# Optimization experiments

Measured on AMD Instinct MI355X. Metric: run time of the kernel, lower is better.

## Reference

```python
import jax, jax.numpy as jnp
import numpy as np

N_NODES = 100000
N_EDGES = 1000000
F_IN = 64
F_HID = 64
F_OUT = 2
NUM_GRAPHS = 64


def setup_inputs() -> dict:
    key = jax.random.key(0)
    ks = jax.random.split(key, 8)
    x = jax.random.normal(ks[0], (N_NODES, F_IN), dtype=jnp.float32)
    edge_index = jax.random.randint(ks[1], (2, N_EDGES), 0, N_NODES, dtype=jnp.int32)
    batch = jnp.sort(jax.random.randint(ks[2], (N_NODES,), 0, NUM_GRAPHS, dtype=jnp.int32))
    s1 = 1.0 / np.sqrt(F_IN)
    s2 = 1.0 / np.sqrt(F_HID)
    W1 = jax.random.normal(ks[3], (F_IN, F_HID), dtype=jnp.float32) * s1
    W2 = jax.random.normal(ks[4], (F_HID, F_HID), dtype=jnp.float32) * s2
    W3 = jax.random.normal(ks[5], (F_HID, F_HID), dtype=jnp.float32) * s2
    Wlin = jax.random.normal(ks[6], (F_HID, F_OUT), dtype=jnp.float32) * s2
    return {
        "x": x, "edge_index": edge_index, "batch": batch,
        "W1": W1, "b1": jnp.zeros((F_HID,), jnp.float32),
        "W2": W2, "b2": jnp.zeros((F_HID,), jnp.float32),
        "W3": W3, "b3": jnp.zeros((F_HID,), jnp.float32),
        "Wlin": Wlin, "blin": jnp.zeros((F_OUT,), jnp.float32),
    }


def _gcn_norm(edge_index, n_nodes):
    # add self-loops, compute symmetric D^-1/2 (A+I) D^-1/2 edge weights
    loops = jnp.arange(n_nodes, dtype=edge_index.dtype)
    src = jnp.concatenate([edge_index[0], loops])  # message source j
    dst = jnp.concatenate([edge_index[1], loops])  # aggregation target i
    deg = jax.ops.segment_sum(jnp.ones_like(dst, dtype=jnp.float32), dst,
                              num_segments=n_nodes)
    dinv = jnp.where(deg > 0, jax.lax.rsqrt(deg), 0.0)
    norm = dinv[src] * dinv[dst]  # [E+N]
    return src, dst, norm


def _gcn_conv(h, W, b, src, dst, norm, n_nodes):
    h = h @ W                                    # [N, F] dense transform first (PyG order)
    msg = h[src] * norm[:, None]                 # gather + scale  [E+N, F]
    agg = jax.ops.segment_sum(msg, dst, num_segments=n_nodes)
    return agg + b


def reference(x, edge_index, batch, W1, b1, W2, b2, W3, b3, Wlin, blin):
    n = x.shape[0]
    src, dst, norm = _gcn_norm(edge_index, n)
    h = jax.nn.relu(_gcn_conv(x, W1, b1, src, dst, norm, n))
    h = jax.nn.relu(_gcn_conv(h, W2, b2, src, dst, norm, n))
    h = _gcn_conv(h, W3, b3, src, dst, norm, n)
    # global mean pool over graphs
    sums = jax.ops.segment_sum(h, batch, num_segments=NUM_GRAPHS)        # [G, F]
    cnts = jax.ops.segment_sum(jnp.ones((n,), jnp.float32), batch,
                               num_segments=NUM_GRAPHS)
    pooled = sums / jnp.maximum(cnts, 1.0)[:, None]
    # dropout(p=0.1) is identity in eval mode
    return pooled @ Wlin + blin
```

## Files before the change

kernel.cpp:

```cpp
#include <hip/hip_runtime.h>

#define FDIM 64

typedef unsigned short u16;
typedef unsigned int u32;
typedef float v2f __attribute__((ext_vector_type(2)));

__device__ __forceinline__ u16 f2bf(float x) {
    unsigned int u = __float_as_uint(x);
    return (u16)((u + 0x7fff + ((u >> 16) & 1)) >> 16);
}
__device__ __forceinline__ float bf2f(u16 h) {
    return __uint_as_float(((unsigned int)h) << 16);
}
__device__ __forceinline__ u32 pk_fp8x4(float a, float b, float c, float d) {
    u32 p = __builtin_amdgcn_cvt_pk_fp8_f32(a, b, 0, false);
    p = __builtin_amdgcn_cvt_pk_fp8_f32(c, d, p, true);
    return p;
}


template <bool BF16IN>
__device__ __forceinline__ void mm_tile64(
    const void* __restrict__ ain, const float* __restrict__ bias, int do_relu,
    u32* __restrict__ t, int n, int blk,
    float (*__restrict__ As)[FDIM + 1], float* __restrict__ Ws)
{
    int tid = threadIdx.x;
    int r0 = blk * 64;

    #pragma unroll
    for (int i = 0; i < 4; ++i) {
        int idx = tid + 256 * i;
        int r = idx >> 4;
        int kq = idx & 15;
        float4 v = make_float4(0.f, 0.f, 0.f, 0.f);
        int R = r0 + r;
        if (R < n) {
            if (BF16IN) {
                ushort4 h = ((const ushort4*)ain)[(size_t)R * 16 + kq];
                v.x = bf2f(h.x); v.y = bf2f(h.y); v.z = bf2f(h.z); v.w = bf2f(h.w);
            } else {
                v = ((const float4*)ain)[(size_t)R * 16 + kq];
            }
            if (bias != nullptr) {
                float4 b = ((const float4*)bias)[kq];
                v.x += b.x; v.y += b.y; v.z += b.z; v.w += b.w;
            }
            if (do_relu) {
                v.x = fmaxf(v.x, 0.f); v.y = fmaxf(v.y, 0.f);
                v.z = fmaxf(v.z, 0.f); v.w = fmaxf(v.w, 0.f);
            }
        }
        As[r][kq * 4 + 0] = v.x;
        As[r][kq * 4 + 1] = v.y;
        As[r][kq * 4 + 2] = v.z;
        As[r][kq * 4 + 3] = v.w;
    }
    __syncthreads();

    int rq = tid >> 4;
    int cq = tid & 15;
    float acc[4][4];
    #pragma unroll
    for (int i = 0; i < 4; ++i)
        #pragma unroll
        for (int j = 0; j < 4; ++j) acc[i][j] = 0.f;

    const float4* Ws4 = (const float4*)Ws;
    #pragma unroll 4
    for (int k = 0; k < FDIM; ++k) {
        float4 w = Ws4[k * 16 + cq];
        float a[4];
        #pragma unroll
        for (int i = 0; i < 4; ++i) a[i] = As[rq * 4 + i][k];
        #pragma unroll
        for (int i = 0; i < 4; ++i) {
            acc[i][0] = fmaf(a[i], w.x, acc[i][0]);
            acc[i][1] = fmaf(a[i], w.y, acc[i][1]);
            acc[i][2] = fmaf(a[i], w.z, acc[i][2]);
            acc[i][3] = fmaf(a[i], w.w, acc[i][3]);
        }
    }

    #pragma unroll
    for (int i = 0; i < 4; ++i) {
        int R = r0 + rq * 4 + i;
        if (R < n)
            t[(size_t)R * 16 + cq] =
                pk_fp8x4(acc[i][0], acc[i][1], acc[i][2], acc[i][3]);
    }
}

__global__ __launch_bounds__(256) void k_matmul_h(
    const u16* __restrict__ ain, const float* __restrict__ Wm,
    const float* __restrict__ bias, u32* __restrict__ t, int n)
{
    __shared__ float As[64][FDIM + 1];
    __shared__ float Ws[FDIM * FDIM];
    int tid = threadIdx.x;
    #pragma unroll
    for (int i = 0; i < 4; ++i)
        ((float4*)Ws)[tid + 256 * i] = ((const float4*)Wm)[tid + 256 * i];
    mm_tile64<true>(ain, bias, 1, t, n, blockIdx.x, As, Ws);
}


__global__ __launch_bounds__(256) void k_mm_fill(
    const float* __restrict__ x, const float* __restrict__ W1,
    u32* __restrict__ t,
    const int* __restrict__ src, const int* __restrict__ dst,
    int* __restrict__ cnt, int* __restrict__ csr,
    int n, int E, int cap, int mm_blocks, int fill_chunks)
{
    __shared__ float As[64][FDIM + 1];
    __shared__ float Ws[FDIM * FDIM];

    if ((int)blockIdx.x < mm_blocks) {
        int tid = threadIdx.x;
        #pragma unroll
        for (int i = 0; i < 4; ++i)
            ((float4*)Ws)[tid + 256 * i] = ((const float4*)W1)[tid + 256 * i];
        mm_tile64<false>(x, nullptr, 0, t, n, blockIdx.x, As, Ws);
        return;
    }
    int gb = blockIdx.x - mm_blocks;
    int part = blockIdx.x & 7;
    int chunk = gb >> 3;
    int psz = n >> 3;
    int lo = psz * part;
    int hi = (part == 7) ? n : lo + psz;
    int per = (E + fill_chunks - 1) / fill_chunks;
    int ebeg = chunk * per;
    int eend = ebeg + per; if (eend > E) eend = E;

    int e = ebeg + (int)threadIdx.x;
    for (; e + 1792 < eend; e += 2048) {
        int d[8], s[8], p[8];
        bool kk[8];
        #pragma unroll
        for (int u = 0; u < 8; ++u) d[u] = __builtin_nontemporal_load(&dst[e + 256 * u]);
        #pragma unroll
        for (int u = 0; u < 8; ++u) s[u] = __builtin_nontemporal_load(&src[e + 256 * u]);
        #pragma unroll
        for (int u = 0; u < 8; ++u) kk[u] = (d[u] >= lo) && (d[u] < hi);
        #pragma unroll
        for (int u = 0; u < 8; ++u) { p[u] = 0; if (kk[u]) p[u] = atomicAdd(&cnt[d[u]], 1); }
        #pragma unroll
        for (int u = 0; u < 8; ++u)
            if (kk[u] && p[u] < cap) csr[(size_t)d[u] * cap + p[u]] = s[u];
    }
    for (; e < eend; e += 256) {
        int d = dst[e];
        if (d >= lo && d < hi) {
            int p = atomicAdd(&cnt[d], 1);
            if (p < cap) csr[(size_t)d * cap + p] = src[e];
        }
    }
}


__global__ __launch_bounds__(256) void k_aggregate(
    const int* __restrict__ cnt, const int* __restrict__ csr,
    const u32* __restrict__ t, uint2* __restrict__ aggh, int n, int cap)
{
    int tid = threadIdx.x;
    long long gw = ((long long)blockIdx.x * 256 + tid) >> 6;
    int lane = tid & 63;
    int sub = lane >> 4;
    int li  = lane & 15;
    long long il = gw * 4 + sub;
    if (il >= n) return;
    int i = (int)il;

    int deg = cnt[i];
    float di = rsqrtf((float)deg + 1.0f);
    int m = deg < cap ? deg : cap;

    u32 sp = t[(size_t)i * 16 + li];
    v2f s0 = __builtin_amdgcn_cvt_pk_f32_fp8(sp, false);
    v2f s1 = __builtin_amdgcn_cvt_pk_f32_fp8(sp, true);
    float4 A0 = make_float4(s0.x * di, s0.y * di, s1.x * di, s1.y * di);
    float4 A1 = make_float4(0.f, 0.f, 0.f, 0.f);
    float4 A2 = make_float4(0.f, 0.f, 0.f, 0.f);
    float4 A3 = make_float4(0.f, 0.f, 0.f, 0.f);

    const int* row = csr + (size_t)i * cap;
    int nbase = sub << 4;

    for (int c0 = 0; c0 < m; c0 += 16) {
        int cm = m - c0; if (cm > 16) cm = 16;
        int sv = 0; float dvv = 0.f;
        if (li < cm) {
            sv = __builtin_nontemporal_load(&row[c0 + li]);
            dvv = rsqrtf((float)cnt[sv] + 1.0f);
        }
        int k = 0;
        for (; k + 8 <= cm; k += 8) {
            int jv[8]; float dj[8]; u32 v[8];
            #pragma unroll
            for (int u = 0; u < 8; ++u) {
                jv[u] = __shfl(sv, nbase + k + u);
                dj[u] = __shfl(dvv, nbase + k + u);
            }
            #pragma unroll
            for (int u = 0; u < 8; ++u) v[u] = t[(size_t)jv[u] * 16 + li];
            #pragma unroll
            for (int u = 0; u < 8; ++u) {
                v2f x0 = __builtin_amdgcn_cvt_pk_f32_fp8(v[u], false);
                v2f x1 = __builtin_amdgcn_cvt_pk_f32_fp8(v[u], true);
                float4* Ap = (u & 3) == 0 ? &A0 : (u & 3) == 1 ? &A1 :
                             (u & 3) == 2 ? &A2 : &A3;
                Ap->x = fmaf(x0.x, dj[u], Ap->x);
                Ap->y = fmaf(x0.y, dj[u], Ap->y);
                Ap->z = fmaf(x1.x, dj[u], Ap->z);
                Ap->w = fmaf(x1.y, dj[u], Ap->w);
            }
        }
        if (k + 4 <= cm) {
            int jv[4]; float dj[4]; u32 v[4];
            #pragma unroll
            for (int u = 0; u < 4; ++u) {
                jv[u] = __shfl(sv, nbase + k + u);
                dj[u] = __shfl(dvv, nbase + k + u);
            }
            #pragma unroll
            for (int u = 0; u < 4; ++u) v[u] = t[(size_t)jv[u] * 16 + li];
            #pragma unroll
            for (int u = 0; u < 4; ++u) {
                v2f x0 = __builtin_amdgcn_cvt_pk_f32_fp8(v[u], false);
                v2f x1 = __builtin_amdgcn_cvt_pk_f32_fp8(v[u], true);
                float4* Ap = u == 0 ? &A0 : u == 1 ? &A1 : u == 2 ? &A2 : &A3;
                Ap->x = fmaf(x0.x, dj[u], Ap->x);
                Ap->y = fmaf(x0.y, dj[u], Ap->y);
                Ap->z = fmaf(x1.x, dj[u], Ap->z);
                Ap->w = fmaf(x1.y, dj[u], Ap->w);
            }
            k += 4;
        }
        for (; k < cm; ++k) {
            int j = __shfl(sv, nbase + k);
            float dj = __shfl(dvv, nbase + k);
            u32 vv = t[(size_t)j * 16 + li];
            v2f x0 = __builtin_amdgcn_cvt_pk_f32_fp8(vv, false);
            v2f x1 = __builtin_amdgcn_cvt_pk_f32_fp8(vv, true);
            A0.x = fmaf(x0.x, dj, A0.x);
            A0.y = fmaf(x0.y, dj, A0.y);
            A0.z = fmaf(x1.x, dj, A0.z);
            A0.w = fmaf(x1.y, dj, A0.w);
        }
    }

    float4 O;
    O.x = ((A0.x + A1.x) + (A2.x + A3.x)) * di;
    O.y = ((A0.y + A1.y) + (A2.y + A3.y)) * di;
    O.z = ((A0.z + A1.z) + (A2.z + A3.z)) * di;
    O.w = ((A0.w + A1.w) + (A2.w + A3.w)) * di;
    uint2 pk;
    pk.x = ((u32)f2bf(O.x)) | (((u32)f2bf(O.y)) << 16);
    pk.y = ((u32)f2bf(O.z)) | (((u32)f2bf(O.w)) << 16);
    aggh[(size_t)i * 16 + li] = pk;
}


__global__ __launch_bounds__(256) void k_pool1(
    const u32* __restrict__ aggh, const int* __restrict__ batch,
    float* __restrict__ partial, int n)
{
    int g = blockIdx.x >> 3;
    int part = blockIdx.x & 7;
    int tid = threadIdx.x;

    int lo = 0, hi = n;
    while (lo < hi) { int mid = (lo + hi) >> 1; if (batch[mid] < g) lo = mid + 1; else hi = mid; }
    int start = lo;
    hi = n;
    while (lo < hi) { int mid = (lo + hi) >> 1; if (batch[mid] <= g) lo = mid + 1; else hi = mid; }
    int end = lo;

    int f2 = tid & 31;
    int r = tid >> 5;
    float sx = 0.f, sy = 0.f;
    for (int i = start + part * 8 + r; i < end; i += 64) {
        u32 v = aggh[(size_t)i * 32 + f2];
        sx += __uint_as_float(v << 16);
        sy += __uint_as_float(v & 0xffff0000u);
    }

    __shared__ float redx[8][32];
    __shared__ float redy[8][32];
    redx[r][f2] = sx;
    redy[r][f2] = sy;
    __syncthreads();
    if (tid < 32) {
        float vx = 0.f, vy = 0.f;
        #pragma unroll
        for (int q = 0; q < 8; ++q) { vx += redx[q][tid]; vy += redy[q][tid]; }
        partial[((size_t)g * 8 + part) * 64 + 2 * tid + 0] = vx;
        partial[((size_t)g * 8 + part) * 64 + 2 * tid + 1] = vy;
    }
}

__global__ __launch_bounds__(64) void k_pool2(
    const float* __restrict__ partial, const int* __restrict__ batch,
    const float* __restrict__ b3, const float* __restrict__ Wlin,
    const float* __restrict__ blin, float* __restrict__ out,
    int n, int fout)
{
    int g = blockIdx.x;
    int tid = threadIdx.x;

    int lo = 0, hi = n;
    while (lo < hi) { int mid = (lo + hi) >> 1; if (batch[mid] < g) lo = mid + 1; else hi = mid; }
    int start = lo;
    hi = n;
    while (lo < hi) { int mid = (lo + hi) >> 1; if (batch[mid] <= g) lo = mid + 1; else hi = mid; }
    int cnt = lo - start;

    __shared__ float pooled[64];
    float v = 0.f;
    #pragma unroll
    for (int p = 0; p < 8; ++p) v += partial[((size_t)g * 8 + p) * 64 + tid];
    pooled[tid] = (cnt > 0) ? (v / (float)cnt + b3[tid]) : 0.f;
    __syncthreads();
    if (tid < fout) {
        float o = blin[tid];
        for (int k = 0; k < 64; ++k) o += pooled[k] * Wlin[k * fout + tid];
        out[(size_t)g * fout + tid] = o;
    }
}


extern "C" void kernel_launch(void* const* d_in, const int* in_sizes, int n_in,
                              void* d_out, int out_size, void* d_ws, size_t ws_size,
                              hipStream_t stream) {
    const float* x     = (const float*)d_in[0];
    const int*   ei    = (const int*)d_in[1];
    const int*   batch = (const int*)d_in[2];
    const float* W1 = (const float*)d_in[3];
    const float* b1 = (const float*)d_in[4];
    const float* W2 = (const float*)d_in[5];
    const float* b2 = (const float*)d_in[6];
    const float* W3 = (const float*)d_in[7];
    const float* b3 = (const float*)d_in[8];
    const float* Wl = (const float*)d_in[9];
    const float* bl = (const float*)d_in[10];

    int n = in_sizes[0] / 64;
    int E = in_sizes[1] / 2;
    int fout = in_sizes[10];
    int ngraphs = out_size / fout;

    const int* srcp = ei;
    const int* dstp = ei + E;

    float* ws   = (float*)d_ws;
    u32*   agg  = (u32*)ws;
    u32*   t    = agg + (size_t)n * 32;
    float* partial = (float*)(t + (size_t)n * 16);
    int* cnt    = (int*)(partial + 64 * 8 * 64);
    int* csr    = cnt + n;

    size_t fixed = (size_t)n * 32 * 4 + (size_t)n * 16 * 4 +
                   64 * 8 * 64 * 4 + (size_t)n * 4;
    int cap = 64;
    while (cap > 32 && fixed + (size_t)n * cap * 4 > ws_size) cap -= 8;

    int nb_ag = (int)((((long long)(n + 3) / 4) * 64 + 255) / 256);
    int mm_blocks = (((n + 63) / 64 + 7) / 8) * 8;
    int fill_chunks = 128;

    hipMemsetAsync(cnt, 0, (size_t)n * sizeof(int), stream);
    k_mm_fill<<<mm_blocks + 8 * fill_chunks, 256, 0, stream>>>(
        x, W1, t, srcp, dstp, cnt, csr, n, E, cap, mm_blocks, fill_chunks);

    k_aggregate<<<nb_ag, 256, 0, stream>>>(cnt, csr, t, (uint2*)agg, n, cap);
    k_matmul_h<<<mm_blocks, 256, 0, stream>>>((const u16*)agg, W2, b1, t, n);
    k_aggregate<<<nb_ag, 256, 0, stream>>>(cnt, csr, t, (uint2*)agg, n, cap);
    k_matmul_h<<<mm_blocks, 256, 0, stream>>>((const u16*)agg, W3, b2, t, n);
    k_aggregate<<<nb_ag, 256, 0, stream>>>(cnt, csr, t, (uint2*)agg, n, cap);

    k_pool1<<<ngraphs * 8, 256, 0, stream>>>(agg, batch, partial, n);
    k_pool2<<<ngraphs, 64, 0, stream>>>(partial, batch, b3, Wl, bl, (float*)d_out, n, fout);
}
```

Before: 288.2 us.

## Fuse final aggregation into graph mean-pool and simplify CSR fill partitioning

The third neighbor aggregation is fused into the pooling kernel: each block aggregates nodes of its graph and accumulates directly into per-part float partial sums, which skips writing and re-reading the bf16 aggregate buffer. The CSR fill changes from 8 destination-range partitions, where each edge chunk was scanned by 8 blocks, to a single grid-stride pass over all edges that does atomics directly. Fill blocks are now placed before the matmul blocks. The fused kernel runs only 64*16 blocks, so per-graph load balance and occupancy may be lower than the full-grid aggregate. The unpartitioned fill also loses destination locality for the atomics and CSR writes.

```diff
diff --git a/kernel.cpp b/kernel.cpp
--- a/kernel.cpp
+++ b/kernel.cpp
@@ -111,68 +111,49 @@
     u32* __restrict__ t,
     const int* __restrict__ src, const int* __restrict__ dst,
     int* __restrict__ cnt, int* __restrict__ csr,
-    int n, int E, int cap, int mm_blocks, int fill_chunks)
+    int n, int E, int cap, int fill_blocks)
 {
     __shared__ float As[64][FDIM + 1];
     __shared__ float Ws[FDIM * FDIM];
 
-    if ((int)blockIdx.x < mm_blocks) {
-        int tid = threadIdx.x;
-        #pragma unroll
-        for (int i = 0; i < 4; ++i)
-            ((float4*)Ws)[tid + 256 * i] = ((const float4*)W1)[tid + 256 * i];
-        mm_tile64<false>(x, nullptr, 0, t, n, blockIdx.x, As, Ws);
-        return;
-    }
-    int gb = blockIdx.x - mm_blocks;
-    int part = blockIdx.x & 7;
-    int chunk = gb >> 3;
-    int psz = n >> 3;
-    int lo = psz * part;
-    int hi = (part == 7) ? n : lo + psz;
-    int per = (E + fill_chunks - 1) / fill_chunks;
-    int ebeg = chunk * per;
-    int eend = ebeg + per; if (eend > E) eend = E;
-
-    int e = ebeg + (int)threadIdx.x;
-    for (; e + 1792 < eend; e += 2048) {
-        int d[8], s[8], p[8];
-        bool kk[8];
-        #pragma unroll
-        for (int u = 0; u < 8; ++u) d[u] = __builtin_nontemporal_load(&dst[e + 256 * u]);
-        #pragma unroll
-        for (int u = 0; u < 8; ++u) s[u] = __builtin_nontemporal_load(&src[e + 256 * u]);
-        #pragma unroll
-        for (int u = 0; u < 8; ++u) kk[u] = (d[u] >= lo) && (d[u] < hi);
-        #pragma unroll
-        for (int u = 0; u < 8; ++u) { p[u] = 0; if (kk[u]) p[u] = atomicAdd(&cnt[d[u]], 1); }
-        #pragma unroll
-        for (int u = 0; u < 8; ++u)
-            if (kk[u] && p[u] < cap) csr[(size_t)d[u] * cap + p[u]] = s[u];
-    }
-    for (; e < eend; e += 256) {
-        int d = dst[e];
-        if (d >= lo && d < hi) {
+    if ((int)blockIdx.x < fill_blocks) {
+        int stride = fill_blocks * 256;
+        int e = blockIdx.x * 256 + threadIdx.x;
+        for (; e + 7 * stride < E; e += 8 * stride) {
+            int d[8], s[8], p[8];
+            #pragma unroll
+            for (int u = 0; u < 8; ++u)
+                d[u] = __builtin_nontemporal_load(&dst[e + u * stride]);
+            #pragma unroll
+            for (int u = 0; u < 8; ++u)
+                s[u] = __builtin_nontemporal_load(&src[e + u * stride]);
+            #pragma unroll
+            for (int u = 0; u < 8; ++u) p[u] = atomicAdd(&cnt[d[u]], 1);
+            #pragma unroll
+            for (int u = 0; u < 8; ++u)
+                if (p[u] < cap) csr[(size_t)d[u] * cap + p[u]] = s[u];
+        }
+        for (; e < E; e += stride) {
+            int d = dst[e];
             int p = atomicAdd(&cnt[d], 1);
             if (p < cap) csr[(size_t)d * cap + p] = src[e];
         }
-    }
-}
-
-
-__global__ __launch_bounds__(256) void k_aggregate(
-    const int* __restrict__ cnt, const int* __restrict__ csr,
-    const u32* __restrict__ t, uint2* __restrict__ aggh, int n, int cap)
-{
-    int tid = threadIdx.x;
-    long long gw = ((long long)blockIdx.x * 256 + tid) >> 6;
-    int lane = tid & 63;
-    int sub = lane >> 4;
-    int li  = lane & 15;
-    long long il = gw * 4 + sub;
-    if (il >= n) return;
-    int i = (int)il;
-
+        return;
+    }
+
+    int blk = blockIdx.x - fill_blocks;
+    int tid = threadIdx.x;
+    #pragma unroll
+    for (int i = 0; i < 4; ++i)
+        ((float4*)Ws)[tid + 256 * i] = ((const float4*)W1)[tid + 256 * i];
+    mm_tile64<false>(x, nullptr, 0, t, n, blk, As, Ws);
+}
+
+
+__device__ __forceinline__ float4 agg_node(
+    int i, const int* __restrict__ cnt, const int* __restrict__ csr,
+    const u32* __restrict__ t, int cap, int li, int nbase)
+{
     int deg = cnt[i];
     float di = rsqrtf((float)deg + 1.0f);
     int m = deg < cap ? deg : cap;
@@ -186,7 +167,6 @@
     float4 A3 = make_float4(0.f, 0.f, 0.f, 0.f);
 
     const int* row = csr + (size_t)i * cap;
-    int nbase = sub << 4;
 
     for (int c0 = 0; c0 < m; c0 += 16) {
         int cm = m - c0; if (cm > 16) cm = 16;
@@ -256,6 +236,24 @@
     O.y = ((A0.y + A1.y) + (A2.y + A3.y)) * di;
     O.z = ((A0.z + A1.z) + (A2.z + A3.z)) * di;
     O.w = ((A0.w + A1.w) + (A2.w + A3.w)) * di;
+    return O;
+}
+
+
+__global__ __launch_bounds__(256) void k_aggregate(
+    const int* __restrict__ cnt, const int* __restrict__ csr,
+    const u32* __restrict__ t, uint2* __restrict__ aggh, int n, int cap)
+{
+    int tid = threadIdx.x;
+    long long gw = ((long long)blockIdx.x * 256 + tid) >> 6;
+    int lane = tid & 63;
+    int sub = lane >> 4;
+    int li  = lane & 15;
+    long long il = gw * 4 + sub;
+    if (il >= n) return;
+    int i = (int)il;
+
+    float4 O = agg_node(i, cnt, csr, t, cap, li, sub << 4);
     uint2 pk;
     pk.x = ((u32)f2bf(O.x)) | (((u32)f2bf(O.y)) << 16);
     pk.y = ((u32)f2bf(O.z)) | (((u32)f2bf(O.w)) << 16);
@@ -263,12 +261,13 @@
 }
 
 
-__global__ __launch_bounds__(256) void k_pool1(
-    const u32* __restrict__ aggh, const int* __restrict__ batch,
-    float* __restrict__ partial, int n)
-{
-    int g = blockIdx.x >> 3;
-    int part = blockIdx.x & 7;
+__global__ __launch_bounds__(256) void k_agg_pool(
+    const int* __restrict__ cnt, const int* __restrict__ csr,
+    const u32* __restrict__ t, const int* __restrict__ batch,
+    float* __restrict__ partial, int n, int cap, int npart)
+{
+    int g = blockIdx.x / npart;
+    int part = blockIdx.x - g * npart;
     int tid = threadIdx.x;
 
     int lo = 0, hi = n;
@@ -278,26 +277,28 @@
     while (lo < hi) { int mid = (lo + hi) >> 1; if (batch[mid] <= g) lo = mid + 1; else hi = mid; }
     int end = lo;
 
-    int f2 = tid & 31;
-    int r = tid >> 5;
-    float sx = 0.f, sy = 0.f;
-    for (int i = start + part * 8 + r; i < end; i += 64) {
-        u32 v = aggh[(size_t)i * 32 + f2];
-        sx += __uint_as_float(v << 16);
-        sy += __uint_as_float(v & 0xffff0000u);
-    }
-
-    __shared__ float redx[8][32];
-    __shared__ float redy[8][32];
-    redx[r][f2] = sx;
-    redy[r][f2] = sy;
+    int group = tid >> 4;
+    int li = tid & 15;
+    int lane = tid & 63;
+    int nbase = (lane >> 4) << 4;
+
+    float4 acc = make_float4(0.f, 0.f, 0.f, 0.f);
+    for (int i = start + part * 16 + group; i < end; i += npart * 16) {
+        float4 O = agg_node(i, cnt, csr, t, cap, li, nbase);
+        acc.x += O.x; acc.y += O.y; acc.z += O.z; acc.w += O.w;
+    }
+
+    __shared__ float4 red[16][16];
+    red[group][li] = acc;
     __syncthreads();
-    if (tid < 32) {
-        float vx = 0.f, vy = 0.f;
+    if (tid < 16) {
+        float4 s = make_float4(0.f, 0.f, 0.f, 0.f);
         #pragma unroll
-        for (int q = 0; q < 8; ++q) { vx += redx[q][tid]; vy += redy[q][tid]; }
-        partial[((size_t)g * 8 + part) * 64 + 2 * tid + 0] = vx;
-        partial[((size_t)g * 8 + part) * 64 + 2 * tid + 1] = vy;
+        for (int q = 0; q < 16; ++q) {
+            s.x += red[q][tid].x; s.y += red[q][tid].y;
+            s.z += red[q][tid].z; s.w += red[q][tid].w;
+        }
+        ((float4*)partial)[((size_t)g * npart + part) * 16 + tid] = s;
     }
 }
 
@@ -305,7 +306,7 @@
     const float* __restrict__ partial, const int* __restrict__ batch,
     const float* __restrict__ b3, const float* __restrict__ Wlin,
     const float* __restrict__ blin, float* __restrict__ out,
-    int n, int fout)
+    int n, int fout, int npart)
 {
     int g = blockIdx.x;
     int tid = threadIdx.x;
@@ -319,8 +320,8 @@
 
     __shared__ float pooled[64];
     float v = 0.f;
-    #pragma unroll
-    for (int p = 0; p < 8; ++p) v += partial[((size_t)g * 8 + p) * 64 + tid];
+    for (int p = 0; p < npart; ++p)
+        v += partial[((size_t)g * npart + p) * 64 + tid];
     pooled[tid] = (cnt > 0) ? (v / (float)cnt + b3[tid]) : 0.f;
     __syncthreads();
     if (tid < fout) {
@@ -354,32 +355,34 @@
     const int* srcp = ei;
     const int* dstp = ei + E;
 
+    const int npart = 16;
+
     float* ws   = (float*)d_ws;
     u32*   agg  = (u32*)ws;
     u32*   t    = agg + (size_t)n * 32;
     float* partial = (float*)(t + (size_t)n * 16);
-    int* cnt    = (int*)(partial + 64 * 8 * 64);
+    int* cnt    = (int*)(partial + 64 * npart * 64);
     int* csr    = cnt + n;
 
     size_t fixed = (size_t)n * 32 * 4 + (size_t)n * 16 * 4 +
-                   64 * 8 * 64 * 4 + (size_t)n * 4;
+                   64 * npart * 64 * 4 + (size_t)n * 4;
     int cap = 64;
     while (cap > 32 && fixed + (size_t)n * cap * 4 > ws_size) cap -= 8;
 
     int nb_ag = (int)((((long long)(n + 3) / 4) * 64 + 255) / 256);
-    int mm_blocks = (((n + 63) / 64 + 7) / 8) * 8;
-    int fill_chunks = 128;
+    int mm_blocks = (n + 63) / 64;
+    int fill_blocks = 256;
 
     hipMemsetAsync(cnt, 0, (size_t)n * sizeof(int), stream);
-    k_mm_fill<<<mm_blocks + 8 * fill_chunks, 256, 0, stream>>>(
-        x, W1, t, srcp, dstp, cnt, csr, n, E, cap, mm_blocks, fill_chunks);
+    k_mm_fill<<<fill_blocks + mm_blocks, 256, 0, stream>>>(
+        x, W1, t, srcp, dstp, cnt, csr, n, E, cap, fill_blocks);
 
     k_aggregate<<<nb_ag, 256, 0, stream>>>(cnt, csr, t, (uint2*)agg, n, cap);
     k_matmul_h<<<mm_blocks, 256, 0, stream>>>((const u16*)agg, W2, b1, t, n);
     k_aggregate<<<nb_ag, 256, 0, stream>>>(cnt, csr, t, (uint2*)agg, n, cap);
     k_matmul_h<<<mm_blocks, 256, 0, stream>>>((const u16*)agg, W3, b2, t, n);
-    k_aggregate<<<nb_ag, 256, 0, stream>>>(cnt, csr, t, (uint2*)agg, n, cap);
-
-    k_pool1<<<ngraphs * 8, 256, 0, stream>>>(agg, batch, partial, n);
-    k_pool2<<<ngraphs, 64, 0, stream>>>(partial, batch, b3, Wl, bl, (float*)d_out, n, fout);
-}
+    k_agg_pool<<<ngraphs * npart, 256, 0, stream>>>(cnt, csr, t, batch,
+                                                    partial, n, cap, npart);
+    k_pool2<<<ngraphs, 64, 0, stream>>>(partial, batch, b3, Wl, bl,
+                                        (float*)d_out, n, fout, npart);
+}
```

Result: faster. 282.1 us (-2.1%).
